# Performance work log

Measured on AMD Instinct MI355X. Metric: run time of the kernel, lower is better.

Reference implementation:

```python
import jax, jax.numpy as jnp
import numpy as np

N_NODES = 100000
DEG = 16
N_EDGES = N_NODES * DEG
R = 8          # num_relations
C_IN = 64
C_OUT = 64


def setup_inputs() -> dict:
    key = jax.random.key(0)
    k1, k2, k3, k4 = jax.random.split(key, 4)
    x_feat = jax.random.normal(k1, (N_NODES, C_IN), dtype=jnp.float32)
    # xavier-ish scale for weight
    scale = (6.0 / (C_IN + C_OUT)) ** 0.5
    weight = jax.random.uniform(k2, (R + 1, C_IN, C_OUT), dtype=jnp.float32,
                                minval=-scale, maxval=scale)
    bias = jnp.zeros((C_OUT,), dtype=jnp.float32)
    # fixed-degree CSR: row_ptr = arange * DEG
    csr_row_ptr = (jnp.arange(N_NODES + 1, dtype=jnp.int64) * DEG)
    csr_col_ind = jax.random.randint(k3, (N_EDGES,), 0, N_NODES, dtype=jnp.int64)
    edge_type = jax.random.randint(k4, (N_EDGES,), 0, R, dtype=jnp.int64)
    return {"x_feat": x_feat, "weight": weight, "bias": bias,
            "csr_row_ptr": csr_row_ptr, "csr_col_ind": csr_col_ind,
            "edge_type": edge_type, "dup_count": DEG}


def reference(x_feat, weight, bias, csr_row_ptr, csr_col_ind, edge_type, dup_count):
    n_dst = csr_row_ptr.shape[0] - 1
    n_edges = csr_col_ind.shape[0]
    # per-edge destination node ids from CSR row pointer
    degrees = jnp.diff(csr_row_ptr)
    dst = jnp.repeat(jnp.arange(n_dst, dtype=csr_row_ptr.dtype), degrees,
                     total_repeat_length=n_edges)
    # segment id = (dst, relation) pair
    seg = (dst * R + edge_type).astype(jnp.int32)
    gathered = x_feat[csr_col_ind]                                  # [E, C_in]
    sums = jax.ops.segment_sum(gathered, seg, num_segments=n_dst * R)  # [N*R, C_in]
    counts = jax.ops.segment_sum(jnp.ones((n_edges,), x_feat.dtype), seg,
                                 num_segments=n_dst * R)
    # mean aggregation per (node, relation); empty relations -> 0
    agg = sums / jnp.maximum(counts, 1.0)[:, None]
    agg = agg.reshape(n_dst, R * x_feat.shape[1])                   # [N, R*C_in]
    # root (self) feature appended last, matching weight[-1]
    x_agg = jnp.concatenate([agg, x_feat[:n_dst]], axis=1)          # [N, (R+1)*C_in]
    y = x_agg @ weight.reshape(-1, weight.shape[-1]) + bias         # [N, C_out]
    return y
```

## Files before the change

### kernel.cpp

```cpp
#include <hip/hip_runtime.h>
#include <hip/hip_bf16.h>

#define R_REL   8
#define C_DIM   64
#define K_DIM   576
#define KT_N    18
#define CT_N    4
#define TILE_M  16
#define K_PAD   584

typedef __attribute__((ext_vector_type(8))) short bf16x8;
typedef __attribute__((ext_vector_type(4))) float f32x4;
typedef __attribute__((ext_vector_type(2))) unsigned u32x2;

static __device__ __forceinline__ unsigned short f2bf(float f) {
    union { float f; unsigned u; } v; v.f = f;
    unsigned r = v.u + 0x7FFFu + ((v.u >> 16) & 1u);
    return (unsigned short)(r >> 16);
}
static __device__ __forceinline__ float bf2f(unsigned u16) {
    union { unsigned u; float f; } v; v.u = u16 << 16;
    return v.f;
}

__global__ void pack_w_kernel(const float* __restrict__ w, unsigned int* __restrict__ wf) {
    int t = blockIdx.x * blockDim.x + threadIdx.x;
    if (t >= KT_N * CT_N * 64) return;
    int lane = t & 63;
    int ct   = (t >> 6) & 3;
    int kt   = t >> 8;
    int row0 = kt * 32 + (lane >> 4) * 8;
    int col  = ct * 16 + (lane & 15);
    unsigned short v[8];
#pragma unroll
    for (int j = 0; j < 8; ++j)
        v[j] = f2bf(w[(row0 + j) * C_DIM + col]);
    uint4 o;
    o.x = (unsigned)v[0] | ((unsigned)v[1] << 16);
    o.y = (unsigned)v[2] | ((unsigned)v[3] << 16);
    o.z = (unsigned)v[4] | ((unsigned)v[5] << 16);
    o.w = (unsigned)v[6] | ((unsigned)v[7] << 16);
    ((uint4*)wf)[t] = o;
}

__global__ void cvt_x_kernel(const float* __restrict__ x, unsigned short* __restrict__ xb,
                             int n4) {
    int i = blockIdx.x * blockDim.x + threadIdx.x;
    if (i >= n4) return;
    float4 v = ((const float4*)x)[i];
    ushort4 o;
    o.x = f2bf(v.x); o.y = f2bf(v.y); o.z = f2bf(v.z); o.w = f2bf(v.w);
    ((ushort4*)xb)[i] = o;
}

#define ACCUM_SWITCH(RELV, VV)                                  \
    switch (RELV) {                                             \
        case 0: s0 += (VV); ++c0; break;                        \
        case 1: s1 += (VV); ++c1; break;                        \
        case 2: s2 += (VV); ++c2; break;                        \
        case 3: s3 += (VV); ++c3; break;                        \
        case 4: s4 += (VV); ++c4; break;                        \
        case 5: s5 += (VV); ++c5; break;                        \
        case 6: s6 += (VV); ++c6; break;                        \
        default: s7 += (VV); ++c7; break;                       \
    }

template<int USE_BF>
__global__ __launch_bounds__(256, 4) void rgcn_kernel(
    const float* __restrict__ x_feat,
    const unsigned short* __restrict__ xb,
    const float* __restrict__ bias,
    const int*   __restrict__ row_ptr,
    const int*   __restrict__ col_ind,
    const int*   __restrict__ edge_type,
    const unsigned short* __restrict__ wfrag,
    float* __restrict__ out,
    int n_nodes)
{
    __shared__ __align__(16) unsigned short xa[TILE_M][K_PAD];
    __shared__ __align__(16) int            col_lds[4][64];
    __shared__ __align__(8)  unsigned char  rel_lds[4][64];
    __shared__ __align__(4)  unsigned short inv_lds[4][32];

    const int tid   = threadIdx.x;
    const int lane  = tid & 63;
    const int w     = tid >> 6;
    const int m0    = blockIdx.x * TILE_M;
    const int nbase = m0 + w * 4;

    const int n_l   = nbase + (lane >> 4);
    const bool v_l  = n_l < n_nodes;
    int rp0   = v_l ? row_ptr[n_l]     : 0;
    int rp1   = v_l ? row_ptr[n_l + 1] : 0;
    int deg_l = v_l ? (rp1 - rp0) : -1;
    int col_l = col_ind[rp0 + (lane & 15)];
    int rel_l = edge_type[rp0 + (lane & 15)];

    const bool fast = USE_BF && (__ballot(deg_l == 16) == ~0ull);

    if (fast) {
        col_lds[w][lane] = col_l;
        rel_lds[w][lane] = (unsigned char)rel_l;
        unsigned long long bsel = 0;
#pragma unroll
        for (int r = 0; r < 8; ++r) {
            unsigned long long b = __ballot(rel_l == r);
            bsel = ((lane & 7) == r) ? b : bsel;
        }
        if (lane < 32) {
            int nd  = (lane >> 3) & 3;
            int cnt = __popcll(bsel & (0xFFFFull << (nd * 16)));
            inv_lds[w][lane] = f2bf(1.0f / (float)(cnt > 0 ? cnt : 1));
        }

        u32x2 selfv = *(const u32x2*)(xb + (size_t)(nbase + (lane >> 4)) * C_DIM
                                      + (lane & 15) * 4);
        *(u32x2*)&xa[w * 4 + (lane >> 4)][8 * C_DIM + (lane & 15) * 4] = selfv;

        const int q8 = (lane >> 4) * 8;
        int4 c0a = *(const int4*)&col_lds[w][q8];
        int4 c0b = *(const int4*)&col_lds[w][q8 + 4];
        int4 c1a = *(const int4*)&col_lds[w][32 + q8];
        int4 c1b = *(const int4*)&col_lds[w][32 + q8 + 4];
        int src0[8] = {c0a.x, c0a.y, c0a.z, c0a.w, c0b.x, c0b.y, c0b.z, c0b.w};
        int src1[8] = {c1a.x, c1a.y, c1a.z, c1a.w, c1b.x, c1b.y, c1b.z, c1b.w};

        const unsigned short* xbase = xb + (lane & 15);
        unsigned bw0[4][4], bw1[4][4];
#pragma unroll
        for (int d = 0; d < 4; ++d) {
            const unsigned short* pLo0 = xbase + (size_t)src0[2 * d]     * C_DIM;
            const unsigned short* pHi0 = xbase + (size_t)src0[2 * d + 1] * C_DIM;
            const unsigned short* pLo1 = xbase + (size_t)src1[2 * d]     * C_DIM;
            const unsigned short* pHi1 = xbase + (size_t)src1[2 * d + 1] * C_DIM;
#pragma unroll
            for (int g = 0; g < 4; ++g) {
                unsigned lo0 = pLo0[g * 16], hi0 = pHi0[g * 16];
                unsigned lo1 = pLo1[g * 16], hi1 = pHi1[g * 16];
                bw0[g][d] = lo0 | (hi0 << 16);
                bw1[g][d] = lo1 | (hi1 << 16);
            }
        }

        const unsigned rl    = lane & 7;
        const bool     hi_ok = (lane >> 5) == ((lane & 15) >> 3);
#pragma unroll
        for (int pr = 0; pr < 2; ++pr) {
            const unsigned char* relp = &rel_lds[w][pr * 32 + q8];
            unsigned rlo = *(const unsigned*)relp;
            unsigned rhi = *(const unsigned*)(relp + 4);
            unsigned inv16 = inv_lds[w][(pr * 2 + ((lane & 15) >> 3)) * 8 + (lane & 7)];
            unsigned invg  = hi_ok ? inv16 : 0u;
            unsigned af[4];
#pragma unroll
            for (int d = 0; d < 4; ++d) {
                unsigned wrd = (d < 2) ? rlo : rhi;
                unsigned b0 = (wrd >> ((d & 1) * 16)) & 0xFFu;
                unsigned b1 = (wrd >> ((d & 1) * 16 + 8)) & 0xFFu;
                af[d] = (b0 == rl ? invg : 0u) | ((b1 == rl ? invg : 0u) << 16);
            }
            union { unsigned u[4]; bf16x8 v; } au;
            au.u[0] = af[0]; au.u[1] = af[1]; au.u[2] = af[2]; au.u[3] = af[3];

#pragma unroll
            for (int g = 0; g < 4; ++g) {
                union { unsigned u[4]; bf16x8 v; } bu;
                if (pr == 0) {
                    bu.u[0] = bw0[g][0]; bu.u[1] = bw0[g][1];
                    bu.u[2] = bw0[g][2]; bu.u[3] = bw0[g][3];
                } else {
                    bu.u[0] = bw1[g][0]; bu.u[1] = bw1[g][1];
                    bu.u[2] = bw1[g][2]; bu.u[3] = bw1[g][3];
                }
                f32x4 dacc = __builtin_amdgcn_mfma_f32_16x16x32_bf16(
                                 au.v, bu.v, (f32x4){0.f, 0.f, 0.f, 0.f}, 0, 0, 0);
#pragma unroll
                for (int reg = 0; reg < 4; ++reg) {
                    int m = (lane >> 4) * 4 + reg;
                    xa[w * 4 + pr * 2 + (m >> 3)][(m & 7) * C_DIM + g * 16 + (lane & 15)]
                        = f2bf(dacc[reg]);
                }
            }
        }
    } else {
        for (int mi_ = 0; mi_ < 4; ++mi_) {
            const int mi = w * 4 + mi_;
            const int n  = nbase + mi_;
            const int sdeg  = __builtin_amdgcn_readlane(deg_l, mi_ * 16);
            const int sbase = __builtin_amdgcn_readlane(rp0,   mi_ * 16);
            if (sdeg < 0) {
                for (int k = lane; k < K_DIM; k += 64) xa[mi][k] = 0;
                continue;
            }
            float s0=0,s1=0,s2=0,s3=0,s4=0,s5=0,s6=0,s7=0;
            int   c0=0,c1=0,c2=0,c3=0,c4=0,c5=0,c6=0,c7=0;
            for (int e = 0; e < sdeg; ++e) {
                int src = col_ind[sbase + e];
                int rlv = edge_type[sbase + e];
                float vv = USE_BF ? bf2f(xb[(size_t)src * C_DIM + lane])
                                  : x_feat[(size_t)src * C_DIM + lane];
                ACCUM_SWITCH(rlv, vv)
            }
            xa[mi][0*C_DIM+lane] = f2bf(s0 * __fdividef(1.0f, (float)(c0>0?c0:1)));
            xa[mi][1*C_DIM+lane] = f2bf(s1 * __fdividef(1.0f, (float)(c1>0?c1:1)));
            xa[mi][2*C_DIM+lane] = f2bf(s2 * __fdividef(1.0f, (float)(c2>0?c2:1)));
            xa[mi][3*C_DIM+lane] = f2bf(s3 * __fdividef(1.0f, (float)(c3>0?c3:1)));
            xa[mi][4*C_DIM+lane] = f2bf(s4 * __fdividef(1.0f, (float)(c4>0?c4:1)));
            xa[mi][5*C_DIM+lane] = f2bf(s5 * __fdividef(1.0f, (float)(c5>0?c5:1)));
            xa[mi][6*C_DIM+lane] = f2bf(s6 * __fdividef(1.0f, (float)(c6>0?c6:1)));
            xa[mi][7*C_DIM+lane] = f2bf(s7 * __fdividef(1.0f, (float)(c7>0?c7:1)));
            xa[mi][8*C_DIM+lane] = USE_BF ? (unsigned short)xb[(size_t)n * C_DIM + lane]
                                          : f2bf(x_feat[(size_t)n * C_DIM + lane]);
        }
    }
    __syncthreads();

    const int ct   = w;
    f32x4 acc = {0,0,0,0};
    const int arow = lane & 15;
    const int kgrp2 = lane >> 4;
    const bf16x8* wf8 = (const bf16x8*)wfrag;
#pragma unroll
    for (int kt = 0; kt < KT_N; ++kt) {
        bf16x8 a = *(const bf16x8*)&xa[arow][kt * 32 + kgrp2 * 8];
        acc = __builtin_amdgcn_mfma_f32_16x16x32_bf16(a, wf8[(kt*4 + ct)*64 + lane], acc, 0,0,0);
    }

    const int col   = ct * 16 + (lane & 15);
    const float b   = bias[col];
    const int rbase = (lane >> 4) * 4;
#pragma unroll
    for (int j = 0; j < 4; ++j) {
        int n = m0 + rbase + j;
        if (n < n_nodes)
            out[n * C_DIM + col] = acc[j] + b;
    }
}

extern "C" void kernel_launch(void* const* d_in, const int* in_sizes, int n_in,
                              void* d_out, int out_size, void* d_ws, size_t ws_size,
                              hipStream_t stream) {
    const float* x_feat    = (const float*)d_in[0];
    const float* weight    = (const float*)d_in[1];
    const float* bias      = (const float*)d_in[2];
    const int*   row_ptr   = (const int*)d_in[3];
    const int*   col_ind   = (const int*)d_in[4];
    const int*   edge_type = (const int*)d_in[5];
    float* out = (float*)d_out;

    const int n_nodes = in_sizes[3] - 1;
    const int nblocks = (n_nodes + TILE_M - 1) / TILE_M;

    unsigned int* wfrag = (unsigned int*)d_ws;
    const size_t wf_bytes = (size_t)KT_N * CT_N * 64 * 16;
    const size_t xb_bytes = (size_t)n_nodes * C_DIM * 2;

    pack_w_kernel<<<(KT_N * CT_N * 64 + 255) / 256, 256, 0, stream>>>(weight, wfrag);

    if (ws_size >= wf_bytes + xb_bytes) {
        unsigned short* xb = (unsigned short*)((char*)d_ws + wf_bytes);
        int n4 = n_nodes * C_DIM / 4;
        cvt_x_kernel<<<(n4 + 255) / 256, 256, 0, stream>>>(x_feat, xb, n4);
        rgcn_kernel<1><<<nblocks, 256, 0, stream>>>(x_feat, xb, bias, row_ptr, col_ind,
                                                    edge_type, (const unsigned short*)d_ws,
                                                    out, n_nodes);
    } else {
        rgcn_kernel<0><<<nblocks, 256, 0, stream>>>(x_feat, nullptr, bias, row_ptr, col_ind,
                                                    edge_type, (const unsigned short*)d_ws,
                                                    out, n_nodes);
    }
}
```

Measured before the change: 59.30 us.

## Interleave bf16 feature layout so each lane gathers 8 contiguous bytes per edge

The bf16 copy of x is stored with channels interleaved (channel c*4+g holds original channel g*16+c), so each lane fetches one 8-byte vector per neighbor instead of four scattered 2-byte loads. The weight packing permutes the root-feature rows to match the permuted self-feature slot, and the fallback path adjusts its indexing. It also raises the launch-bounds occupancy hint from 4 to 8 blocks per CU, which may force register spilling. The permuted layout is meant to cut gather instruction count and memory transactions, at the cost of a strided read pattern in the conversion kernel.

```diff
diff --git a/kernel.cpp b/kernel.cpp
--- a/kernel.cpp
+++ b/kernel.cpp
@@ -12,6 +12,7 @@
 typedef __attribute__((ext_vector_type(8))) short bf16x8;
 typedef __attribute__((ext_vector_type(4))) float f32x4;
 typedef __attribute__((ext_vector_type(2))) unsigned u32x2;
+
 
 static __device__ __forceinline__ unsigned short f2bf(float f) {
     union { float f; unsigned u; } v; v.f = f;
@@ -33,8 +34,11 @@
     int col  = ct * 16 + (lane & 15);
     unsigned short v[8];
 #pragma unroll
-    for (int j = 0; j < 8; ++j)
-        v[j] = f2bf(w[(row0 + j) * C_DIM + col]);
+    for (int j = 0; j < 8; ++j) {
+        int rk = row0 + j;
+        int wr = (rk < 512) ? rk : 512 + ((rk - 512) & 3) * 16 + ((rk - 512) >> 2);
+        v[j] = f2bf(w[wr * C_DIM + col]);
+    }
     uint4 o;
     o.x = (unsigned)v[0] | ((unsigned)v[1] << 16);
     o.y = (unsigned)v[2] | ((unsigned)v[3] << 16);
@@ -44,13 +48,17 @@
 }
 
 __global__ void cvt_x_kernel(const float* __restrict__ x, unsigned short* __restrict__ xb,
-                             int n4) {
-    int i = blockIdx.x * blockDim.x + threadIdx.x;
-    if (i >= n4) return;
-    float4 v = ((const float4*)x)[i];
+                             int total) {
+    int t = blockIdx.x * blockDim.x + threadIdx.x;
+    if (t >= total) return;
+    int n = t >> 4, c = t & 15;
+    const float* xr = x + (size_t)n * C_DIM + c;
     ushort4 o;
-    o.x = f2bf(v.x); o.y = f2bf(v.y); o.z = f2bf(v.z); o.w = f2bf(v.w);
-    ((ushort4*)xb)[i] = o;
+    o.x = f2bf(xr[0]);
+    o.y = f2bf(xr[16]);
+    o.z = f2bf(xr[32]);
+    o.w = f2bf(xr[48]);
+    *(ushort4*)(xb + (size_t)n * C_DIM + c * 4) = o;
 }
 
 #define ACCUM_SWITCH(RELV, VV)                                  \
@@ -66,7 +74,7 @@
     }
 
 template<int USE_BF>
-__global__ __launch_bounds__(256, 4) void rgcn_kernel(
+__global__ __launch_bounds__(256, 8) void rgcn_kernel(
     const float* __restrict__ x_feat,
     const unsigned short* __restrict__ xb,
     const float* __restrict__ bias,
@@ -125,21 +133,29 @@
         int src0[8] = {c0a.x, c0a.y, c0a.z, c0a.w, c0b.x, c0b.y, c0b.z, c0b.w};
         int src1[8] = {c1a.x, c1a.y, c1a.z, c1a.w, c1b.x, c1b.y, c1b.z, c1b.w};
 
-        const unsigned short* xbase = xb + (lane & 15);
+        const unsigned short* xbase = xb + (lane & 15) * 4;
+        u32x2 gv0[8], gv1[8];
+#pragma unroll
+        for (int e = 0; e < 8; ++e) {
+            gv0[e] = *(const u32x2*)(xbase + (size_t)src0[e] * C_DIM);
+            gv1[e] = *(const u32x2*)(xbase + (size_t)src1[e] * C_DIM);
+        }
+
         unsigned bw0[4][4], bw1[4][4];
 #pragma unroll
         for (int d = 0; d < 4; ++d) {
-            const unsigned short* pLo0 = xbase + (size_t)src0[2 * d]     * C_DIM;
-            const unsigned short* pHi0 = xbase + (size_t)src0[2 * d + 1] * C_DIM;
-            const unsigned short* pLo1 = xbase + (size_t)src1[2 * d]     * C_DIM;
-            const unsigned short* pHi1 = xbase + (size_t)src1[2 * d + 1] * C_DIM;
-#pragma unroll
-            for (int g = 0; g < 4; ++g) {
-                unsigned lo0 = pLo0[g * 16], hi0 = pHi0[g * 16];
-                unsigned lo1 = pLo1[g * 16], hi1 = pHi1[g * 16];
-                bw0[g][d] = lo0 | (hi0 << 16);
-                bw1[g][d] = lo1 | (hi1 << 16);
-            }
+            unsigned lx = gv0[2*d].x, hx = gv0[2*d+1].x;
+            unsigned ly = gv0[2*d].y, hy = gv0[2*d+1].y;
+            bw0[0][d] = (lx & 0xFFFFu) | (hx << 16);
+            bw0[1][d] = (lx >> 16)     | (hx & 0xFFFF0000u);
+            bw0[2][d] = (ly & 0xFFFFu) | (hy << 16);
+            bw0[3][d] = (ly >> 16)     | (hy & 0xFFFF0000u);
+            lx = gv1[2*d].x; hx = gv1[2*d+1].x;
+            ly = gv1[2*d].y; hy = gv1[2*d+1].y;
+            bw1[0][d] = (lx & 0xFFFFu) | (hx << 16);
+            bw1[1][d] = (lx >> 16)     | (hx & 0xFFFF0000u);
+            bw1[2][d] = (ly & 0xFFFFu) | (hy << 16);
+            bw1[3][d] = (ly >> 16)     | (hy & 0xFFFF0000u);
         }
 
         const unsigned rl    = lane & 7;
@@ -194,10 +210,11 @@
             }
             float s0=0,s1=0,s2=0,s3=0,s4=0,s5=0,s6=0,s7=0;
             int   c0=0,c1=0,c2=0,c3=0,c4=0,c5=0,c6=0,c7=0;
+            const int ich = (lane & 15) * 4 + (lane >> 4);
             for (int e = 0; e < sdeg; ++e) {
                 int src = col_ind[sbase + e];
                 int rlv = edge_type[sbase + e];
-                float vv = USE_BF ? bf2f(xb[(size_t)src * C_DIM + lane])
+                float vv = USE_BF ? bf2f(xb[(size_t)src * C_DIM + ich])
                                   : x_feat[(size_t)src * C_DIM + lane];
                 ACCUM_SWITCH(rlv, vv)
             }
@@ -210,7 +227,8 @@
             xa[mi][6*C_DIM+lane] = f2bf(s6 * __fdividef(1.0f, (float)(c6>0?c6:1)));
             xa[mi][7*C_DIM+lane] = f2bf(s7 * __fdividef(1.0f, (float)(c7>0?c7:1)));
             xa[mi][8*C_DIM+lane] = USE_BF ? (unsigned short)xb[(size_t)n * C_DIM + lane]
-                                          : f2bf(x_feat[(size_t)n * C_DIM + lane]);
+                                          : f2bf(x_feat[(size_t)n * C_DIM
+                                                        + (lane & 3) * 16 + (lane >> 2)]);
         }
     }
     __syncthreads();
@@ -259,8 +277,8 @@
 
     if (ws_size >= wf_bytes + xb_bytes) {
         unsigned short* xb = (unsigned short*)((char*)d_ws + wf_bytes);
-        int n4 = n_nodes * C_DIM / 4;
-        cvt_x_kernel<<<(n4 + 255) / 256, 256, 0, stream>>>(x_feat, xb, n4);
+        int total = n_nodes * 16;
+        cvt_x_kernel<<<(total + 255) / 256, 256, 0, stream>>>(x_feat, xb, total);
         rgcn_kernel<1><<<nblocks, 256, 0, stream>>>(x_feat, xb, bias, row_ptr, col_ind,
                                                     edge_type, (const unsigned short*)d_ws,
                                                     out, n_nodes);
```

After: 56.44 us. 1.05x faster.
